# Kernel optimization log

Hardware: AMD Instinct MI355X
Metric: run time of the kernel (lower is better)

## Reference

```python
import jax, jax.numpy as jnp
from jax import lax
import numpy as np

B = 16
C1, H1, W1 = 512, 28, 28   # wide_resnet50_2 layer2 @ 224px
C2, H2, W2 = 1024, 14, 14  # wide_resnet50_2 layer3 @ 224px
M = 15000                  # memory bank max size (embedding_max_len)
D = C1 + C2                # 1536
IMG = 224                  # input_size
NUM_NEIGHBORS = 9
SIGMA = 4.0                # anomalib AnomalyMapGenerator default
KS = 2 * int(4.0 * SIGMA + 0.5) + 1  # 33 (kornia kernel-size rule)


def setup_inputs() -> dict:
    key = jax.random.key(0)
    k1, k2, k3 = jax.random.split(key, 3)
    return {
        "feat1": jax.random.normal(k1, (B, C1, H1, W1), dtype=jnp.float32),
        "feat2": jax.random.normal(k2, (B, C2, H2, W2), dtype=jnp.float32),
        "memory_bank": jax.random.normal(k3, (M, D), dtype=jnp.float32),
    }


def _avg_pool3(x):
    # torch.nn.AvgPool2d(3, 1, 1) with count_include_pad=True -> sum window / 9
    s = lax.reduce_window(x, 0.0, lax.add, (1, 1, 3, 3), (1, 1, 1, 1),
                          [(0, 0), (0, 0), (1, 1), (1, 1)])
    return s / 9.0


def _edist(x, y):
    x_norm = jnp.sum(x * x, axis=-1, keepdims=True)
    y_norm = jnp.sum(y * y, axis=-1, keepdims=True)
    res = x_norm - 2.0 * jnp.matmul(x, jnp.swapaxes(y, -2, -1)) + jnp.swapaxes(y_norm, -2, -1)
    return jnp.sqrt(jnp.maximum(res, 0.0))


def _gauss_kernel():
    t = jnp.arange(KS, dtype=jnp.float32) - (KS - 1) / 2.0
    g = jnp.exp(-(t * t) / (2.0 * SIGMA * SIGMA))
    return g / jnp.sum(g)


def _gaussian_blur(x):
    # separable depthwise gaussian blur with reflect padding (kornia GaussianBlur2d)
    g = _gauss_kernel()
    p = KS // 2
    x = jnp.pad(x, ((0, 0), (0, 0), (p, p), (p, p)), mode='reflect')
    dn = ('NCHW', 'OIHW', 'NCHW')
    x = lax.conv_general_dilated(x, g.reshape(1, 1, KS, 1), (1, 1), 'VALID', dimension_numbers=dn)
    x = lax.conv_general_dilated(x, g.reshape(1, 1, 1, KS), (1, 1), 'VALID', dimension_numbers=dn)
    return x


def reference(feat1, feat2, memory_bank):
    # 1. feature pooling + hierarchical embedding concat
    f1 = _avg_pool3(feat1)                                   # [B,512,28,28]
    f2 = _avg_pool3(feat2)                                   # [B,1024,14,14]
    f2 = jax.image.resize(f2, (f2.shape[0], f2.shape[1], H1, W1), 'bilinear')
    emb = jnp.concatenate([f1, f2], axis=1)                  # [B,1536,28,28]
    b, d = emb.shape[0], emb.shape[1]
    e = emb.transpose(0, 2, 3, 1).reshape(-1, d)             # [B*P, D]

    # 2. brute-force 1-NN against memory bank
    dist = _edist(e, memory_bank)                            # [N, M]
    patch_scores = jnp.min(dist, axis=1)                     # [N]
    locations = jnp.argmin(dist, axis=1)                     # [N]
    P = H1 * W1
    ps = patch_scores.reshape(b, P)
    loc = locations.reshape(b, P)

    # 3. image-level anomaly score with num_neighbors=9 re-weighting
    bidx = jnp.arange(b)
    mp = jnp.argmax(ps, axis=1)                              # [B]
    max_feat = e.reshape(b, P, d)[bidx, mp]                  # [B,D]
    score = ps[bidx, mp]                                     # [B]
    nn_index = loc[bidx, mp]                                 # [B]
    nn_sample = memory_bank[nn_index]                        # [B,D]
    d_nb = _edist(nn_sample, memory_bank)                    # [B,M]
    _, support = lax.top_k(-d_nb, NUM_NEIGHBORS)             # [B,9] smallest
    sup_feats = memory_bank[support]                         # [B,9,D]
    d2 = _edist(max_feat[:, None, :], sup_feats)             # [B,1,9]
    weights = (1.0 - jax.nn.softmax(d2[:, 0, :], axis=1))[:, 0]
    pred_score = weights * score                             # [B]

    # 4. anomaly map: upsample patch scores to input size + gaussian blur
    amap = ps.reshape(b, 1, H1, W1)
    amap = jax.image.resize(amap, (b, 1, IMG, IMG), 'bilinear')
    amap = _gaussian_blur(amap)                              # [B,1,224,224]
    return amap, pred_score
```

## Files before the change

kernel.cpp:

```cpp
#include <hip/hip_runtime.h>
#include <stdint.h>

#define B_    16
#define C1_   512
#define C2_   1024
#define H2_   14
#define D_    1536
#define P_    784
#define N_    12544
#define M_    15000
#define MPAD_ 15104
#define MT1_  118
#define MT2_  59
#define NT_   98
#define IMG_  224
#define KS_   33

typedef unsigned short u16;
typedef unsigned int   u32;
typedef unsigned long long u64;

__device__ __forceinline__ u16 f2bf(float x) {
    u32 u = __float_as_uint(x);
    u = u + 0x7fffu + ((u >> 16) & 1u);
    return (u16)(u >> 16);
}
__device__ __forceinline__ float bf2f(u16 h) {
    return __uint_as_float(((u32)h) << 16);
}
__device__ __forceinline__ u32 ordf(float f) {
    u32 u = __float_as_uint(f);
    return (u & 0x80000000u) ? ~u : (u | 0x80000000u);
}
__device__ __forceinline__ float unordf(u32 o) {
    u32 u = (o & 0x80000000u) ? (o ^ 0x80000000u) : ~o;
    return __uint_as_float(u);
}

__global__ void k_pool2(const float* __restrict__ feat2, float* __restrict__ pooled2) {
    int idx = blockIdx.x * 256 + threadIdx.x;
    if (idx >= B_ * C2_ * H2_ * H2_) return;
    int x = idx % 14, y = (idx / 14) % 14, bc = idx / 196;
    const float* src = feat2 + (size_t)bc * 196;
    float s = 0.f;
    for (int dy = -1; dy <= 1; ++dy) {
        int yy = y + dy; if (yy < 0 || yy > 13) continue;
        for (int dx = -1; dx <= 1; ++dx) {
            int xx = x + dx; if (xx < 0 || xx > 13) continue;
            s += src[yy * 14 + xx];
        }
    }
    pooled2[idx] = s * (1.f / 9.f);
}

__global__ __launch_bounds__(192)
void k_bank(const float* __restrict__ bank, u16* __restrict__ Bh,
            u16* __restrict__ Bl, float* __restrict__ ynorm) {
    int m = blockIdx.x, tid = threadIdx.x;
    float nrm = 0.f;
    float v[8];
    if (m < M_) {
        const float4* src = (const float4*)(bank + (size_t)m * D_ + tid * 8);
        float4 a = src[0], b = src[1];
        v[0]=a.x; v[1]=a.y; v[2]=a.z; v[3]=a.w; v[4]=b.x; v[5]=b.y; v[6]=b.z; v[7]=b.w;
#pragma unroll
        for (int i = 0; i < 8; ++i) nrm += v[i] * v[i];
    } else {
#pragma unroll
        for (int i = 0; i < 8; ++i) v[i] = 0.f;
    }
    u32 hw[4], lw[4];
#pragma unroll
    for (int i = 0; i < 4; ++i) {
        u16 h0 = f2bf(v[2*i]),   l0 = f2bf(v[2*i]   - bf2f(h0));
        u16 h1 = f2bf(v[2*i+1]), l1 = f2bf(v[2*i+1] - bf2f(h1));
        hw[i] = (u32)h0 | ((u32)h1 << 16);
        lw[i] = (u32)l0 | ((u32)l1 << 16);
    }
    *(uint4*)(Bh + (size_t)m * D_ + tid * 8) = make_uint4(hw[0], hw[1], hw[2], hw[3]);
    *(uint4*)(Bl + (size_t)m * D_ + tid * 8) = make_uint4(lw[0], lw[1], lw[2], lw[3]);
    __shared__ float red[3];
    for (int off = 32; off; off >>= 1) nrm += __shfl_down(nrm, off, 64);
    int wave = tid >> 6, lane = tid & 63;
    if (lane == 0) red[wave] = nrm;
    __syncthreads();
    if (tid == 0) {
        float t = red[0] + red[1] + red[2];
        ynorm[m] = (m < M_) ? t : __uint_as_float(0x7f800000u);
    }
}

__global__ __launch_bounds__(256)
void k_embed(const float* __restrict__ feat1, const float* __restrict__ pooled2,
             u16* __restrict__ Ah, u16* __restrict__ Al, float* __restrict__ xnorm) {
    __shared__ float sF[3 * 64 * 29];
    __shared__ float xn[28];
    const int tid = threadIdx.x, lane = tid & 63, wave = tid >> 6;
    const int b = blockIdx.x / 28, y = blockIdx.x % 28;
    const int brow = b * P_ + y * 28;
    if (tid < 28) xn[tid] = 0.f;

    float sy = y * 0.5f - 0.25f;
    int iy = (int)floorf(sy);
    float fy = sy - iy;
    int y0 = min(max(iy, 0), 13), y1 = min(max(iy + 1, 0), 13);
    __syncthreads();

    for (int cc = 0; cc < 8; ++cc) {
        for (int j = tid; j < 3 * 64 * 28; j += 256) {
            int x = j % 28, c = (j / 28) % 64, r = j / (28 * 64);
            int yy = y - 1 + r;
            float v = 0.f;
            if (yy >= 0 && yy < 28)
                v = feat1[((size_t)(b * C1_ + cc * 64 + c)) * 784 + yy * 28 + x];
            sF[(r * 64 + c) * 29 + x] = v;
        }
        __syncthreads();
        for (int it = 0; it < 7; ++it) {
            int x = it * 4 + wave, c = lane;
            float s = 0.f;
#pragma unroll
            for (int r = 0; r < 3; ++r) {
                int base = (r * 64 + c) * 29;
                if (x > 0) s += sF[base + x - 1];
                s += sF[base + x];
                if (x < 27) s += sF[base + x + 1];
            }
            float v = s * (1.f / 9.f);
            int col = cc * 64 + c;
            size_t off = (size_t)(brow + x) * D_ + col;
            u16 h = f2bf(v);
            Ah[off] = h; Al[off] = f2bf(v - bf2f(h));
            float vv = v * v;
            for (int m = 1; m < 64; m <<= 1) vv += __shfl_xor(vv, m, 64);
            if (lane == 0) atomicAdd(&xn[x], vv);
        }
        __syncthreads();
    }

    for (int cc = 0; cc < 16; ++cc) {
        for (int it = 0; it < 7; ++it) {
            int x = it * 4 + wave, c = lane;
            const float* sp = pooled2 + ((size_t)(b * C2_ + cc * 64 + c)) * 196;
            float sx = x * 0.5f - 0.25f;
            int ix = (int)floorf(sx);
            float fx = sx - ix;
            int x0 = min(max(ix, 0), 13), x1 = min(max(ix + 1, 0), 13);
            float v = (1.f - fy) * ((1.f - fx) * sp[y0 * 14 + x0] + fx * sp[y0 * 14 + x1])
                    + fy * ((1.f - fx) * sp[y1 * 14 + x0] + fx * sp[y1 * 14 + x1]);
            int col = C1_ + cc * 64 + c;
            size_t off = (size_t)(brow + x) * D_ + col;
            u16 h = f2bf(v);
            Ah[off] = h; Al[off] = f2bf(v - bf2f(h));
            float vv = v * v;
            for (int m = 1; m < 64; m <<= 1) vv += __shfl_xor(vv, m, 64);
            if (lane == 0) atomicAdd(&xn[x], vv);
        }
    }
    __syncthreads();
    if (tid < 28) xnorm[brow + tid] = xn[tid];
}

typedef __bf16 bf16x8 __attribute__((ext_vector_type(8)));
typedef float  f32x4  __attribute__((ext_vector_type(4)));
typedef float  f32x16 __attribute__((ext_vector_type(16)));

__global__ __launch_bounds__(256, 2)
void k_gemm1(const u16* __restrict__ Ah, const u16* __restrict__ Bh,
             const float* __restrict__ ynorm, float* __restrict__ partf) {
    __shared__ u16 sA[128 * 32];
    __shared__ u16 sB[256 * 32];
    __shared__ float smin[128][2];

    const int tid = threadIdx.x, lane = tid & 63, wave = tid >> 6;
    const int GM = 4, nig = GM * NT_;
    const int grp = blockIdx.x / nig, rem = blockIdx.x - grp * nig;
    const int first = grp * GM;
    const int gsz = (MT2_ - first) < GM ? (MT2_ - first) : GM;
    const int mt = first + rem % gsz;
    const int pt = rem / gsz;
    const int p0 = pt * 128, m0 = mt * 256;

    f32x16 acc[2][4];
#pragma unroll
    for (int i = 0; i < 2; ++i)
#pragma unroll
        for (int j = 0; j < 4; ++j)
#pragma unroll
            for (int e = 0; e < 16; ++e) acc[i][j][e] = 0.f;

    const int srow = lane >> 2;
    const int schunk8 = ((lane & 3) ^ ((lane >> 3) & 3)) * 8;
    const int wr = (wave >> 1) * 64, wc = (wave & 1) * 128;
    const int rA = lane & 31, kh = lane >> 5;
    const int rsw = (lane >> 1) & 3;

    for (int kt = 0; kt < 48; ++kt) {
        const int k0 = kt * 32;
#pragma unroll
        for (int s = 0; s < 2; ++s) {
            const int span = wave * 2 + s;
            const int row = span * 16 + srow;
            const u16* ga = Ah + (size_t)(p0 + row) * D_ + k0 + schunk8;
            __builtin_amdgcn_global_load_lds((const __attribute__((address_space(1))) void*)ga,
                (__attribute__((address_space(3))) void*)&sA[span * 512], 16, 0, 0);
        }
#pragma unroll
        for (int s = 0; s < 4; ++s) {
            const int span = wave * 4 + s;
            const int row = span * 16 + srow;
            const u16* gb = Bh + (size_t)(m0 + row) * D_ + k0 + schunk8;
            __builtin_amdgcn_global_load_lds((const __attribute__((address_space(1))) void*)gb,
                (__attribute__((address_space(3))) void*)&sB[span * 512], 16, 0, 0);
        }
        __syncthreads();
        bf16x8 af[2][2], bfr[2][4];
#pragma unroll
        for (int ks = 0; ks < 2; ++ks) {
            const int slot = ((ks * 2 + kh) ^ rsw) * 8;
#pragma unroll
            for (int ti = 0; ti < 2; ++ti)
                af[ks][ti] = *(const bf16x8*)&sA[(wr + ti * 32 + rA) * 32 + slot];
#pragma unroll
            for (int tj = 0; tj < 4; ++tj)
                bfr[ks][tj] = *(const bf16x8*)&sB[(wc + tj * 32 + rA) * 32 + slot];
        }
#pragma unroll
        for (int ks = 0; ks < 2; ++ks)
#pragma unroll
            for (int ti = 0; ti < 2; ++ti)
#pragma unroll
                for (int tj = 0; tj < 4; ++tj)
                    acc[ti][tj] = __builtin_amdgcn_mfma_f32_32x32x16_bf16(
                        af[ks][ti], bfr[ks][tj], acc[ti][tj], 0, 0, 0);
        __syncthreads();
    }

    const int c32 = lane & 31;
    float yn[4];
#pragma unroll
    for (int tj = 0; tj < 4; ++tj) yn[tj] = ynorm[m0 + wc + tj * 32 + c32];
#pragma unroll
    for (int ti = 0; ti < 2; ++ti) {
#pragma unroll
        for (int reg = 0; reg < 16; ++reg) {
            const int rloc = wr + ti * 32 + (reg & 3) + 8 * (reg >> 2) + 4 * kh;
            float v = __uint_as_float(0x7f800000u);
#pragma unroll
            for (int tj = 0; tj < 4; ++tj)
                v = fminf(v, yn[tj] - 2.0f * acc[ti][tj][reg]);
#pragma unroll
            for (int msk = 1; msk < 32; msk <<= 1)
                v = fminf(v, __shfl_xor(v, msk, 64));
            if (c32 == 0) smin[rloc][wave & 1] = v;
        }
    }
    __syncthreads();
    if (tid < 128)
        partf[(size_t)mt * N_ + p0 + tid] = fminf(smin[tid][0], smin[tid][1]);
}

__global__ void k_reduce(const float* __restrict__ partf, const float* __restrict__ xnorm,
                         float* __restrict__ ps) {
    int n = blockIdx.x * 128 + threadIdx.x;
    float best = __uint_as_float(0x7f800000u);
    for (int t = 0; t < MT2_; ++t)
        best = fminf(best, partf[(size_t)t * N_ + n]);
    ps[n] = sqrtf(fmaxf(best + xnorm[n], 0.f));
}

__global__ void k_cand(const float* __restrict__ ps, int* __restrict__ candrow) {
    int b = blockIdx.x, tid = threadIdx.x;
    __shared__ u64 red[4];
    u64 prev = ~0ull;
    for (int j = 0; j < 8; ++j) {
        u64 best = 0;
        for (int p = tid; p < P_; p += 256) {
            u64 pk = ((u64)ordf(ps[b * P_ + p]) << 32) | (u32)(~(u32)p);
            if (pk < prev && pk > best) best = pk;
        }
        for (int msk = 1; msk < 64; msk <<= 1) {
            u64 o = __shfl_xor(best, msk, 64);
            best = o > best ? o : best;
        }
        int wave = tid >> 6, lane = tid & 63;
        if (lane == 0) red[wave] = best;
        __syncthreads();
        u64 m = red[0];
        for (int w = 1; w < 4; ++w) m = red[w] > m ? red[w] : m;
        if (tid == 0) candrow[b * 8 + j] = b * P_ + (int)(~(u32)m);
        prev = m;
        __syncthreads();
    }
}

__global__ __launch_bounds__(256)
void k_gexact(const u16* __restrict__ Ah, const u16* __restrict__ Al,
              const u16* __restrict__ Bh, const u16* __restrict__ Bl,
              const float* __restrict__ ynorm, const int* __restrict__ candrow,
              u64* __restrict__ parte) {
    __shared__ u16 sA[2][128 * 32];
    __shared__ u16 sB[2][128 * 32];
    __shared__ u64 smin[128][2];
    __shared__ int scand[128];

    const int tid = threadIdx.x;
    const int lane = tid & 63, wave = tid >> 6;
    const int mt = blockIdx.x;
    const int m0 = mt * 128;
    if (tid < 128) scand[tid] = candrow[tid];

    f32x16 acc[2][2];
#pragma unroll
    for (int i = 0; i < 2; ++i)
#pragma unroll
        for (int j = 0; j < 2; ++j)
#pragma unroll
            for (int e = 0; e < 16; ++e) acc[i][j][e] = 0.f;

    const int srow = lane >> 2;
    const int scol = ((lane & 3) ^ ((lane >> 3) & 3)) * 8;
    const int wr = (wave >> 1) * 64, wc = (wave & 1) * 64;
    const int rA = lane & 31;
    const int sw = (lane >> 1) & 3;
    __syncthreads();

    for (int kt = 0; kt < 48; ++kt) {
        const int k0 = kt * 32;
#pragma unroll
        for (int s = 0; s < 2; ++s) {
            const int slab = wave * 2 + s;
            const int row = slab * 16 + srow;
            const int grow = scand[row];
            const u16* ga = Ah + (size_t)grow * D_ + k0 + scol;
            __builtin_amdgcn_global_load_lds((const __attribute__((address_space(1))) void*)ga,
                (__attribute__((address_space(3))) void*)&sA[0][slab * 512], 16, 0, 0);
            const u16* ga2 = Al + (size_t)grow * D_ + k0 + scol;
            __builtin_amdgcn_global_load_lds((const __attribute__((address_space(1))) void*)ga2,
                (__attribute__((address_space(3))) void*)&sA[1][slab * 512], 16, 0, 0);
            const u16* gb = Bh + (size_t)(m0 + row) * D_ + k0 + scol;
            __builtin_amdgcn_global_load_lds((const __attribute__((address_space(1))) void*)gb,
                (__attribute__((address_space(3))) void*)&sB[0][slab * 512], 16, 0, 0);
            const u16* gb2 = Bl + (size_t)(m0 + row) * D_ + k0 + scol;
            __builtin_amdgcn_global_load_lds((const __attribute__((address_space(1))) void*)gb2,
                (__attribute__((address_space(3))) void*)&sB[1][slab * 512], 16, 0, 0);
        }
        __syncthreads();
#pragma unroll
        for (int ks = 0; ks < 2; ++ks) {
            const int co = ((ks * 2 + (lane >> 5)) ^ sw) * 8;
            bf16x8 ah0 = *(const bf16x8*)&sA[0][(wr + rA) * 32 + co];
            bf16x8 ah1 = *(const bf16x8*)&sA[0][(wr + 32 + rA) * 32 + co];
            bf16x8 al0 = *(const bf16x8*)&sA[1][(wr + rA) * 32 + co];
            bf16x8 al1 = *(const bf16x8*)&sA[1][(wr + 32 + rA) * 32 + co];
            bf16x8 bh0 = *(const bf16x8*)&sB[0][(wc + rA) * 32 + co];
            bf16x8 bh1 = *(const bf16x8*)&sB[0][(wc + 32 + rA) * 32 + co];
            bf16x8 bl0 = *(const bf16x8*)&sB[1][(wc + rA) * 32 + co];
            bf16x8 bl1 = *(const bf16x8*)&sB[1][(wc + 32 + rA) * 32 + co];
            acc[0][0] = __builtin_amdgcn_mfma_f32_32x32x16_bf16(ah0, bh0, acc[0][0], 0, 0, 0);
            acc[0][1] = __builtin_amdgcn_mfma_f32_32x32x16_bf16(ah0, bh1, acc[0][1], 0, 0, 0);
            acc[1][0] = __builtin_amdgcn_mfma_f32_32x32x16_bf16(ah1, bh0, acc[1][0], 0, 0, 0);
            acc[1][1] = __builtin_amdgcn_mfma_f32_32x32x16_bf16(ah1, bh1, acc[1][1], 0, 0, 0);
            acc[0][0] = __builtin_amdgcn_mfma_f32_32x32x16_bf16(ah0, bl0, acc[0][0], 0, 0, 0);
            acc[0][1] = __builtin_amdgcn_mfma_f32_32x32x16_bf16(ah0, bl1, acc[0][1], 0, 0, 0);
            acc[1][0] = __builtin_amdgcn_mfma_f32_32x32x16_bf16(ah1, bl0, acc[1][0], 0, 0, 0);
            acc[1][1] = __builtin_amdgcn_mfma_f32_32x32x16_bf16(ah1, bl1, acc[1][1], 0, 0, 0);
            acc[0][0] = __builtin_amdgcn_mfma_f32_32x32x16_bf16(al0, bh0, acc[0][0], 0, 0, 0);
            acc[0][1] = __builtin_amdgcn_mfma_f32_32x32x16_bf16(al0, bh1, acc[0][1], 0, 0, 0);
            acc[1][0] = __builtin_amdgcn_mfma_f32_32x32x16_bf16(al1, bh0, acc[1][0], 0, 0, 0);
            acc[1][1] = __builtin_amdgcn_mfma_f32_32x32x16_bf16(al1, bh1, acc[1][1], 0, 0, 0);
        }
        __syncthreads();
    }

    const int wrB = wave >> 1, wcB = wave & 1;
    const int half = lane >> 5, c32 = lane & 31;
    float yn[2];
    yn[0] = ynorm[m0 + wcB * 64 + c32];
    yn[1] = ynorm[m0 + wcB * 64 + 32 + c32];
#pragma unroll
    for (int ti = 0; ti < 2; ++ti) {
#pragma unroll
        for (int reg = 0; reg < 16; ++reg) {
            const int rloc = wrB * 64 + ti * 32 + 4 * half + (reg & 3) + 8 * (reg >> 2);
            u64 best = ~0ull;
#pragma unroll
            for (int tj = 0; tj < 2; ++tj) {
                float v = yn[tj] - 2.0f * acc[ti][tj][reg];
                u32 col = (u32)(m0 + wcB * 64 + tj * 32 + c32);
                u64 pk = ((u64)ordf(v) << 32) | col;
                best = pk < best ? pk : best;
            }
#pragma unroll
            for (int msk = 1; msk < 32; msk <<= 1) {
                u64 o = __shfl_xor(best, msk, 64);
                best = o < best ? o : best;
            }
            if (c32 == 0) smin[rloc][wcB] = best;
        }
    }
    __syncthreads();
    if (tid < 128) {
        u64 a = smin[tid][0], b = smin[tid][1];
        parte[(size_t)mt * 128 + tid] = a < b ? a : b;
    }
}

__global__ void k_pick(const u64* __restrict__ parte, const float* __restrict__ xnorm,
                       const int* __restrict__ candrow, int* __restrict__ mprow,
                       int* __restrict__ nnidx, float* __restrict__ score) {
    __shared__ float sps[128];
    __shared__ int sloc[128];
    int i = threadIdx.x;
    u64 best = ~0ull;
    for (int t = 0; t < MT1_; ++t) {
        u64 v = parte[(size_t)t * 128 + i];
        best = v < best ? v : best;
    }
    float val = unordf((u32)(best >> 32)) + xnorm[candrow[i]];
    sps[i] = sqrtf(fmaxf(val, 0.f));
    sloc[i] = (int)(u32)best;
    __syncthreads();
    if (i < B_) {
        float bs = -1.f; int bj = 0; int brw = 1 << 30;
        for (int j = 0; j < 8; ++j) {
            int idx = i * 8 + j;
            float v = sps[idx];
            int row = candrow[idx];
            if (v > bs || (v == bs && row < brw)) { bs = v; bj = idx; brw = row; }
        }
        mprow[i] = brw;
        nnidx[i] = sloc[bj];
        score[i] = bs;
    }
}

__global__ void k_dnb(const float* __restrict__ bank, const float* __restrict__ ynorm,
                      const int* __restrict__ nnidx, float* __restrict__ dnb) {
    int wave = threadIdx.x >> 6, lane = threadIdx.x & 63;
    int m = blockIdx.x * 4 + wave;
    if (m >= M_) return;
    const float4* br = (const float4*)(bank + (size_t)m * D_);
    float acc[B_];
#pragma unroll
    for (int b = 0; b < B_; ++b) acc[b] = 0.f;
#pragma unroll
    for (int p = 0; p < 6; ++p) {
        float4 c = br[p * 64 + lane];
#pragma unroll
        for (int b = 0; b < B_; ++b) {
            const float4* nr = (const float4*)(bank + (size_t)nnidx[b] * D_);
            float4 a = nr[p * 64 + lane];
            acc[b] += a.x * c.x + a.y * c.y + a.z * c.z + a.w * c.w;
        }
    }
    float ym = ynorm[m];
    float keep = 0.f;
#pragma unroll
    for (int b = 0; b < B_; ++b) {
        float v = acc[b];
        for (int msk = 1; msk < 64; msk <<= 1) v += __shfl_xor(v, msk, 64);
        if (lane == b) keep = v;
    }
    if (lane < B_) {
        float ynn = ynorm[nnidx[lane]];
        dnb[lane * M_ + m] = sqrtf(fmaxf(ynn - 2.f * keep + ym, 0.f));
    }
}

__global__ void k_top9a(const float* __restrict__ dnb, u64* __restrict__ cand9) {
    int blk = blockIdx.x;
    int b = blk >> 3, ch = blk & 7;
    int base = ch * 1875;
    int tid = threadIdx.x;
    __shared__ u64 red[4];
    u64 prev = 0;
    for (int p = 0; p < 9; ++p) {
        u64 best = ~0ull;
        for (int i = tid; i < 1875; i += 256) {
            float v = dnb[b * M_ + base + i];
            u64 pk = ((u64)ordf(v) << 32) | (u32)(base + i);
            if (pk > prev && pk < best) best = pk;
        }
        for (int msk = 1; msk < 64; msk <<= 1) {
            u64 o = __shfl_xor(best, msk, 64);
            best = o < best ? o : best;
        }
        int wave = tid >> 6, lane = tid & 63;
        if (lane == 0) red[wave] = best;
        __syncthreads();
        u64 m = red[0];
        for (int w = 1; w < 4; ++w) m = red[w] < m ? red[w] : m;
        if (tid == 0) cand9[blk * 9 + p] = m;
        prev = m;
        __syncthreads();
    }
}
__global__ void k_top9b(const u64* __restrict__ cand9, int* __restrict__ support) {
    int b = blockIdx.x, lane = threadIdx.x;
    u64 v0 = lane < 72 ? cand9[b * 72 + lane] : ~0ull;
    u64 v1 = (lane + 64) < 72 ? cand9[b * 72 + lane + 64] : ~0ull;
    u64 prev = 0;
    for (int p = 0; p < 9; ++p) {
        u64 best = ~0ull;
        if (v0 > prev && v0 < best) best = v0;
        if (v1 > prev && v1 < best) best = v1;
        for (int msk = 1; msk < 64; msk <<= 1) {
            u64 o = __shfl_xor(best, msk, 64);
            best = o < best ? o : best;
        }
        if (lane == 0) support[b * 9 + p] = (int)(u32)best;
        prev = best;
    }
}

__global__ void k_final(const u16* __restrict__ Ah, const u16* __restrict__ Al,
                        const float* __restrict__ bank, const float* __restrict__ ynorm,
                        const float* __restrict__ xnorm, const int* __restrict__ mprow,
                        const int* __restrict__ support, const float* __restrict__ score,
                        float* __restrict__ out_score) {
    int b = blockIdx.x;
    int wave = threadIdx.x >> 6, lane = threadIdx.x & 63;
    __shared__ float d2s[9];
    int row = mprow[b];
    float xn = xnorm[row];
    for (int s = wave; s < 9; s += 4) {
        int sup = support[b * 9 + s];
        float acc = 0.f;
        for (int p = 0; p < 24; ++p) {
            int k = p * 64 + lane;
            float e = bf2f(Ah[(size_t)row * D_ + k]) + bf2f(Al[(size_t)row * D_ + k]);
            acc += e * bank[(size_t)sup * D_ + k];
        }
        for (int msk = 1; msk < 64; msk <<= 1) acc += __shfl_xor(acc, msk, 64);
        if (lane == 0) d2s[s] = sqrtf(fmaxf(xn - 2.f * acc + ynorm[sup], 0.f));
    }
    __syncthreads();
    if (threadIdx.x == 0) {
        float mx = d2s[0];
        for (int i = 1; i < 9; ++i) mx = fmaxf(mx, d2s[i]);
        float den = 0.f;
        for (int i = 0; i < 9; ++i) den += expf(d2s[i] - mx);
        float w = 1.f - expf(d2s[0] - mx) / den;
        out_score[b] = w * score[b];
    }
}

__global__ void k_upsample(const float* __restrict__ ps, float* __restrict__ U) {
    int idx = blockIdx.x * 256 + threadIdx.x;
    if (idx >= B_ * IMG_ * IMG_) return;
    int x = idx % IMG_, y = (idx / IMG_) % IMG_, b = idx / (IMG_ * IMG_);
    float sx = x * 0.125f - 0.4375f, sy = y * 0.125f - 0.4375f;
    int ix = (int)floorf(sx), iy = (int)floorf(sy);
    float fx = sx - ix, fy = sy - iy;
    int x0 = min(max(ix, 0), 27), x1 = min(max(ix + 1, 0), 27);
    int y0 = min(max(iy, 0), 27), y1 = min(max(iy + 1, 0), 27);
    const float* p = ps + b * P_;
    U[idx] = (1.f - fy) * ((1.f - fx) * p[y0 * 28 + x0] + fx * p[y0 * 28 + x1])
           + fy * ((1.f - fx) * p[y1 * 28 + x0] + fx * p[y1 * 28 + x1]);
}

__global__ void k_blurh(const float* __restrict__ U, float* __restrict__ T) {
    __shared__ float g[KS_];
    __shared__ float gs;
    int tid = threadIdx.x;
    if (tid < KS_) { float d = tid - 16.f; g[tid] = expf(-(d * d) / 32.0f); }
    __syncthreads();
    if (tid == 0) { float s = 0.f; for (int i = 0; i < KS_; ++i) s += g[i]; gs = 1.f / s; }
    __syncthreads();
    int idx = blockIdx.x * 256 + tid;
    if (idx >= B_ * IMG_ * IMG_) return;
    int x = idx % IMG_, rowbase = idx - x;
    float a = 0.f;
    for (int t = 0; t < KS_; ++t) {
        int xx = x + t - 16;
        xx = xx < 0 ? -xx : (xx > 223 ? 446 - xx : xx);
        a += g[t] * U[rowbase + xx];
    }
    T[idx] = a * gs;
}
__global__ void k_blurv(const float* __restrict__ T, float* __restrict__ out) {
    __shared__ float g[KS_];
    __shared__ float gs;
    int tid = threadIdx.x;
    if (tid < KS_) { float d = tid - 16.f; g[tid] = expf(-(d * d) / 32.0f); }
    __syncthreads();
    if (tid == 0) { float s = 0.f; for (int i = 0; i < KS_; ++i) s += g[i]; gs = 1.f / s; }
    __syncthreads();
    int idx = blockIdx.x * 256 + tid;
    if (idx >= B_ * IMG_ * IMG_) return;
    int x = idx % IMG_, y = (idx / IMG_) % IMG_, b = idx / (IMG_ * IMG_);
    float a = 0.f;
    for (int t = 0; t < KS_; ++t) {
        int yy = y + t - 16;
        yy = yy < 0 ? -yy : (yy > 223 ? 446 - yy : yy);
        a += g[t] * T[(b * IMG_ + yy) * IMG_ + x];
    }
    out[idx] = a * gs;
}

extern "C" void kernel_launch(void* const* d_in, const int* in_sizes, int n_in,
                              void* d_out, int out_size, void* d_ws, size_t ws_size,
                              hipStream_t stream) {
    const float* feat1 = (const float*)d_in[0];
    const float* feat2 = (const float*)d_in[1];
    const float* bank  = (const float*)d_in[2];
    float* out = (float*)d_out;
    char* ws = (char*)d_ws;

    size_t o = 0;
    u16* Ah = (u16*)(ws + o); o += (size_t)N_ * D_ * 2;
    u16* Al = (u16*)(ws + o); o += (size_t)N_ * D_ * 2;
    size_t o_Bh = o;
    u16* Bh = (u16*)(ws + o); o += (size_t)MPAD_ * D_ * 2;
    u16* Bl = (u16*)(ws + o); o += (size_t)MPAD_ * D_ * 2;
    size_t o_scr = o;
    float* pooled2 = (float*)(ws + o_scr);
    float* partf   = (float*)(ws + o_scr);
    size_t r1 = (size_t)MT2_ * N_ * 4, r2 = (size_t)B_ * C2_ * 196 * 4;
    o += (r1 > r2 ? r1 : r2);
    float* xnorm = (float*)(ws + o); o += (size_t)N_ * 4;
    float* ynorm = (float*)(ws + o); o += (size_t)MPAD_ * 4;
    float* ps    = (float*)(ws + o); o += (size_t)N_ * 4;
    int* candrow = (int*)(ws + o);   o += 512;
    u64* parte   = (u64*)(ws + o);   o += (size_t)MT1_ * 128 * 8;
    float* dnb   = (float*)(ws + o); o += (size_t)B_ * M_ * 4;
    u64* cand9   = (u64*)(ws + o);   o += 128 * 9 * 8;
    int*   mprow = (int*)(ws + o);   o += 64;
    int*   nnidx = (int*)(ws + o);   o += 64;
    float* score = (float*)(ws + o); o += 64;
    int* support = (int*)(ws + o);   o += 9 * B_ * 4;
    float* U = (float*)(ws + o_Bh);
    float* T = (float*)(ws + o_Bh + (size_t)B_ * IMG_ * IMG_ * 4);

    k_pool2<<<(B_ * C2_ * H2_ * H2_ + 255) / 256, 256, 0, stream>>>(feat2, pooled2);
    k_bank<<<MPAD_, 192, 0, stream>>>(bank, Bh, Bl, ynorm);
    k_embed<<<B_ * 28, 256, 0, stream>>>(feat1, pooled2, Ah, Al, xnorm);
    k_gemm1<<<MT2_ * NT_, 256, 0, stream>>>(Ah, Bh, ynorm, partf);
    k_reduce<<<NT_, 128, 0, stream>>>(partf, xnorm, ps);
    k_cand<<<B_, 256, 0, stream>>>(ps, candrow);
    k_gexact<<<MT1_, 256, 0, stream>>>(Ah, Al, Bh, Bl, ynorm, candrow, parte);
    k_pick<<<1, 128, 0, stream>>>(parte, xnorm, candrow, mprow, nnidx, score);
    k_dnb<<<(M_ + 3) / 4, 256, 0, stream>>>(bank, ynorm, nnidx, dnb);
    k_top9a<<<128, 256, 0, stream>>>(dnb, cand9);
    k_top9b<<<B_, 64, 0, stream>>>(cand9, support);
    k_final<<<B_, 256, 0, stream>>>(Ah, Al, bank, ynorm, xnorm, mprow, support, score,
                                    out + (size_t)B_ * IMG_ * IMG_);
    k_upsample<<<(B_ * IMG_ * IMG_ + 255) / 256, 256, 0, stream>>>(ps, U);
    k_blurh<<<(B_ * IMG_ * IMG_ + 255) / 256, 256, 0, stream>>>(U, T);
    k_blurv<<<(B_ * IMG_ * IMG_ + 255) / 256, 256, 0, stream>>>(T, out);
}
```

Before: 1.255 ms.

## Double-buffer gemm1 LDS tiles and split exact-GEMM K across blocks

The main bf16 GEMM now double-buffers its shared-memory tiles, issuing loads for the next K step before computing on the current one and dropping one barrier per iteration. The exact candidate GEMM is split along K into four slices on a 2D grid, which raises its block count from 118 to 472. Each slice writes raw partial dot products to a workspace buffer. A new k_pickc kernel sums the slices, applies the norms and finds the per-candidate minimum. This adds an extra kernel launch and about 30 MB of partial-result traffic, and doubles LDS use in gemm1, which may lower occupancy.

```diff
diff --git a/kernel.cpp b/kernel.cpp
--- a/kernel.cpp
+++ b/kernel.cpp
@@ -162,14 +162,17 @@
 }
 
 typedef __bf16 bf16x8 __attribute__((ext_vector_type(8)));
-typedef float  f32x4  __attribute__((ext_vector_type(4)));
 typedef float  f32x16 __attribute__((ext_vector_type(16)));
+
+#define GLD16(dst, src) __builtin_amdgcn_global_load_lds( \
+    (const __attribute__((address_space(1))) void*)(src), \
+    (__attribute__((address_space(3))) void*)(dst), 16, 0, 0)
 
 __global__ __launch_bounds__(256, 2)
 void k_gemm1(const u16* __restrict__ Ah, const u16* __restrict__ Bh,
              const float* __restrict__ ynorm, float* __restrict__ partf) {
-    __shared__ u16 sA[128 * 32];
-    __shared__ u16 sB[256 * 32];
+    __shared__ u16 sA[2][128 * 32];
+    __shared__ u16 sB[2][256 * 32];
     __shared__ float smin[128][2];
 
     const int tid = threadIdx.x, lane = tid & 63, wave = tid >> 6;
@@ -195,35 +198,40 @@
     const int rA = lane & 31, kh = lane >> 5;
     const int rsw = (lane >> 1) & 3;
 
+    const int arow0 = (wave * 2 + 0) * 16 + srow, arow1 = (wave * 2 + 1) * 16 + srow;
+    const u16* gA0 = Ah + (size_t)(p0 + arow0) * D_ + schunk8;
+    const u16* gA1 = Ah + (size_t)(p0 + arow1) * D_ + schunk8;
+    const u16* gB0 = Bh + (size_t)(m0 + (wave * 4 + 0) * 16 + srow) * D_ + schunk8;
+    const u16* gB1 = Bh + (size_t)(m0 + (wave * 4 + 1) * 16 + srow) * D_ + schunk8;
+    const u16* gB2 = Bh + (size_t)(m0 + (wave * 4 + 2) * 16 + srow) * D_ + schunk8;
+    const u16* gB3 = Bh + (size_t)(m0 + (wave * 4 + 3) * 16 + srow) * D_ + schunk8;
+    u16* lA0 = &sA[0][(wave * 2 + 0) * 512]; u16* lA1 = &sA[0][(wave * 2 + 1) * 512];
+    u16* lB0 = &sB[0][(wave * 4 + 0) * 512]; u16* lB1 = &sB[0][(wave * 4 + 1) * 512];
+    u16* lB2 = &sB[0][(wave * 4 + 2) * 512]; u16* lB3 = &sB[0][(wave * 4 + 3) * 512];
+    const size_t bufA = 128 * 32, bufB = 256 * 32;
+
+    GLD16(lA0, gA0); GLD16(lA1, gA1);
+    GLD16(lB0, gB0); GLD16(lB1, gB1); GLD16(lB2, gB2); GLD16(lB3, gB3);
+
     for (int kt = 0; kt < 48; ++kt) {
-        const int k0 = kt * 32;
-#pragma unroll
-        for (int s = 0; s < 2; ++s) {
-            const int span = wave * 2 + s;
-            const int row = span * 16 + srow;
-            const u16* ga = Ah + (size_t)(p0 + row) * D_ + k0 + schunk8;
-            __builtin_amdgcn_global_load_lds((const __attribute__((address_space(1))) void*)ga,
-                (__attribute__((address_space(3))) void*)&sA[span * 512], 16, 0, 0);
-        }
-#pragma unroll
-        for (int s = 0; s < 4; ++s) {
-            const int span = wave * 4 + s;
-            const int row = span * 16 + srow;
-            const u16* gb = Bh + (size_t)(m0 + row) * D_ + k0 + schunk8;
-            __builtin_amdgcn_global_load_lds((const __attribute__((address_space(1))) void*)gb,
-                (__attribute__((address_space(3))) void*)&sB[span * 512], 16, 0, 0);
-        }
-        __syncthreads();
+        const int cur = kt & 1, nxt = cur ^ 1;
+        __syncthreads();
+        if (kt < 47) {
+            const int k1 = (kt + 1) * 32;
+            GLD16(lA0 + nxt * bufA, gA0 + k1); GLD16(lA1 + nxt * bufA, gA1 + k1);
+            GLD16(lB0 + nxt * bufB, gB0 + k1); GLD16(lB1 + nxt * bufB, gB1 + k1);
+            GLD16(lB2 + nxt * bufB, gB2 + k1); GLD16(lB3 + nxt * bufB, gB3 + k1);
+        }
         bf16x8 af[2][2], bfr[2][4];
 #pragma unroll
         for (int ks = 0; ks < 2; ++ks) {
             const int slot = ((ks * 2 + kh) ^ rsw) * 8;
 #pragma unroll
             for (int ti = 0; ti < 2; ++ti)
-                af[ks][ti] = *(const bf16x8*)&sA[(wr + ti * 32 + rA) * 32 + slot];
+                af[ks][ti] = *(const bf16x8*)&sA[cur][(wr + ti * 32 + rA) * 32 + slot];
 #pragma unroll
             for (int tj = 0; tj < 4; ++tj)
-                bfr[ks][tj] = *(const bf16x8*)&sB[(wc + tj * 32 + rA) * 32 + slot];
+                bfr[ks][tj] = *(const bf16x8*)&sB[cur][(wc + tj * 32 + rA) * 32 + slot];
         }
 #pragma unroll
         for (int ks = 0; ks < 2; ++ks)
@@ -233,7 +241,6 @@
                 for (int tj = 0; tj < 4; ++tj)
                     acc[ti][tj] = __builtin_amdgcn_mfma_f32_32x32x16_bf16(
                         af[ks][ti], bfr[ks][tj], acc[ti][tj], 0, 0, 0);
-        __syncthreads();
     }
 
     const int c32 = lane & 31;
@@ -297,16 +304,14 @@
 __global__ __launch_bounds__(256)
 void k_gexact(const u16* __restrict__ Ah, const u16* __restrict__ Al,
               const u16* __restrict__ Bh, const u16* __restrict__ Bl,
-              const float* __restrict__ ynorm, const int* __restrict__ candrow,
-              u64* __restrict__ parte) {
+              const int* __restrict__ candrow, float* __restrict__ pdot) {
     __shared__ u16 sA[2][128 * 32];
     __shared__ u16 sB[2][128 * 32];
-    __shared__ u64 smin[128][2];
     __shared__ int scand[128];
 
     const int tid = threadIdx.x;
     const int lane = tid & 63, wave = tid >> 6;
-    const int mt = blockIdx.x;
+    const int mt = blockIdx.x, slice = blockIdx.y;
     const int m0 = mt * 128;
     if (tid < 128) scand[tid] = candrow[tid];
 
@@ -325,25 +330,17 @@
     const int sw = (lane >> 1) & 3;
     __syncthreads();
 
-    for (int kt = 0; kt < 48; ++kt) {
+    for (int kt = slice * 12; kt < slice * 12 + 12; ++kt) {
         const int k0 = kt * 32;
 #pragma unroll
         for (int s = 0; s < 2; ++s) {
             const int slab = wave * 2 + s;
             const int row = slab * 16 + srow;
             const int grow = scand[row];
-            const u16* ga = Ah + (size_t)grow * D_ + k0 + scol;
-            __builtin_amdgcn_global_load_lds((const __attribute__((address_space(1))) void*)ga,
-                (__attribute__((address_space(3))) void*)&sA[0][slab * 512], 16, 0, 0);
-            const u16* ga2 = Al + (size_t)grow * D_ + k0 + scol;
-            __builtin_amdgcn_global_load_lds((const __attribute__((address_space(1))) void*)ga2,
-                (__attribute__((address_space(3))) void*)&sA[1][slab * 512], 16, 0, 0);
-            const u16* gb = Bh + (size_t)(m0 + row) * D_ + k0 + scol;
-            __builtin_amdgcn_global_load_lds((const __attribute__((address_space(1))) void*)gb,
-                (__attribute__((address_space(3))) void*)&sB[0][slab * 512], 16, 0, 0);
-            const u16* gb2 = Bl + (size_t)(m0 + row) * D_ + k0 + scol;
-            __builtin_amdgcn_global_load_lds((const __attribute__((address_space(1))) void*)gb2,
-                (__attribute__((address_space(3))) void*)&sB[1][slab * 512], 16, 0, 0);
+            GLD16(&sA[0][slab * 512], Ah + (size_t)grow * D_ + k0 + scol);
+            GLD16(&sA[1][slab * 512], Al + (size_t)grow * D_ + k0 + scol);
+            GLD16(&sB[0][slab * 512], Bh + (size_t)(m0 + row) * D_ + k0 + scol);
+            GLD16(&sB[1][slab * 512], Bl + (size_t)(m0 + row) * D_ + k0 + scol);
         }
         __syncthreads();
 #pragma unroll
@@ -375,48 +372,54 @@
 
     const int wrB = wave >> 1, wcB = wave & 1;
     const int half = lane >> 5, c32 = lane & 31;
-    float yn[2];
-    yn[0] = ynorm[m0 + wcB * 64 + c32];
-    yn[1] = ynorm[m0 + wcB * 64 + 32 + c32];
+    float* base = pdot + ((size_t)(slice * MT1_ + mt) * 128) * 128;
 #pragma unroll
     for (int ti = 0; ti < 2; ++ti) {
 #pragma unroll
         for (int reg = 0; reg < 16; ++reg) {
             const int rloc = wrB * 64 + ti * 32 + 4 * half + (reg & 3) + 8 * (reg >> 2);
-            u64 best = ~0ull;
-#pragma unroll
-            for (int tj = 0; tj < 2; ++tj) {
-                float v = yn[tj] - 2.0f * acc[ti][tj][reg];
-                u32 col = (u32)(m0 + wcB * 64 + tj * 32 + c32);
-                u64 pk = ((u64)ordf(v) << 32) | col;
-                best = pk < best ? pk : best;
-            }
-#pragma unroll
-            for (int msk = 1; msk < 32; msk <<= 1) {
-                u64 o = __shfl_xor(best, msk, 64);
-                best = o < best ? o : best;
-            }
-            if (c32 == 0) smin[rloc][wcB] = best;
-        }
-    }
-    __syncthreads();
-    if (tid < 128) {
-        u64 a = smin[tid][0], b = smin[tid][1];
-        parte[(size_t)mt * 128 + tid] = a < b ? a : b;
-    }
-}
-
-__global__ void k_pick(const u64* __restrict__ parte, const float* __restrict__ xnorm,
+#pragma unroll
+            for (int tj = 0; tj < 2; ++tj)
+                base[(size_t)rloc * 128 + wcB * 64 + tj * 32 + c32] = acc[ti][tj][reg];
+        }
+    }
+}
+
+__global__ void k_pickc(const float* __restrict__ pdot, const float* __restrict__ ynorm,
+                        u64* __restrict__ candmin) {
+    int i = blockIdx.x, tid = threadIdx.x;
+    __shared__ u64 red[4];
+    u64 best = ~0ull;
+    for (int m = tid; m < MPAD_; m += 256) {
+        float dot = 0.f;
+#pragma unroll
+        for (int s = 0; s < 4; ++s)
+            dot += pdot[((size_t)(s * MT1_ + (m >> 7)) * 128 + i) * 128 + (m & 127)];
+        float v = ynorm[m] - 2.f * dot;
+        u64 pk = ((u64)ordf(v) << 32) | (u32)m;
+        best = pk < best ? pk : best;
+    }
+    for (int msk = 1; msk < 64; msk <<= 1) {
+        u64 o = __shfl_xor(best, msk, 64);
+        best = o < best ? o : best;
+    }
+    int wave = tid >> 6, lane = tid & 63;
+    if (lane == 0) red[wave] = best;
+    __syncthreads();
+    if (tid == 0) {
+        u64 m = red[0];
+        for (int w = 1; w < 4; ++w) m = red[w] < m ? red[w] : m;
+        candmin[i] = m;
+    }
+}
+
+__global__ void k_pick(const u64* __restrict__ candmin, const float* __restrict__ xnorm,
                        const int* __restrict__ candrow, int* __restrict__ mprow,
                        int* __restrict__ nnidx, float* __restrict__ score) {
     __shared__ float sps[128];
     __shared__ int sloc[128];
     int i = threadIdx.x;
-    u64 best = ~0ull;
-    for (int t = 0; t < MT1_; ++t) {
-        u64 v = parte[(size_t)t * 128 + i];
-        best = v < best ? v : best;
-    }
+    u64 best = candmin[i];
     float val = unordf((u32)(best >> 32)) + xnorm[candrow[i]];
     sps[i] = sqrtf(fmaxf(val, 0.f));
     sloc[i] = (int)(u32)best;
@@ -623,7 +626,8 @@
     float* ynorm = (float*)(ws + o); o += (size_t)MPAD_ * 4;
     float* ps    = (float*)(ws + o); o += (size_t)N_ * 4;
     int* candrow = (int*)(ws + o);   o += 512;
-    u64* parte   = (u64*)(ws + o);   o += (size_t)MT1_ * 128 * 8;
+    float* pdot  = (float*)(ws + o); o += (size_t)4 * MT1_ * 128 * 128 * 4;
+    u64* candmin = (u64*)(ws + o);   o += 128 * 8;
     float* dnb   = (float*)(ws + o); o += (size_t)B_ * M_ * 4;
     u64* cand9   = (u64*)(ws + o);   o += 128 * 9 * 8;
     int*   mprow = (int*)(ws + o);   o += 64;
@@ -639,8 +643,9 @@
     k_gemm1<<<MT2_ * NT_, 256, 0, stream>>>(Ah, Bh, ynorm, partf);
     k_reduce<<<NT_, 128, 0, stream>>>(partf, xnorm, ps);
     k_cand<<<B_, 256, 0, stream>>>(ps, candrow);
-    k_gexact<<<MT1_, 256, 0, stream>>>(Ah, Al, Bh, Bl, ynorm, candrow, parte);
-    k_pick<<<1, 128, 0, stream>>>(parte, xnorm, candrow, mprow, nnidx, score);
+    k_gexact<<<dim3(MT1_, 4), 256, 0, stream>>>(Ah, Al, Bh, Bl, candrow, pdot);
+    k_pickc<<<128, 256, 0, stream>>>(pdot, ynorm, candmin);
+    k_pick<<<1, 128, 0, stream>>>(candmin, xnorm, candrow, mprow, nnidx, score);
     k_dnb<<<(M_ + 3) / 4, 256, 0, stream>>>(bank, ynorm, nnidx, dnb);
     k_top9a<<<128, 256, 0, stream>>>(dnb, cand9);
     k_top9b<<<B_, 64, 0, stream>>>(cand9, support);
```

Result: slower. 1.322 ms (+5.4%).
